# Performance work log

Hardware: AMD Instinct MI355X
Metric: run time of the kernel (lower is better)

## Reference

```python
import jax, jax.numpy as jnp
import numpy as np

N = 100000      # nodes
E = 1600000     # edges
R = 8           # relations
D_IN = 64
D_H = 64
D_OUT = 64
G = 64          # graphs in batch


def setup_inputs() -> dict:
    key = jax.random.key(0)
    ks = jax.random.split(key, 10)
    x = jax.random.normal(ks[0], (N, D_IN), dtype=jnp.float32)
    edge_index = jax.random.randint(ks[1], (2, E), 0, N, dtype=jnp.int32)
    edge_type = jax.random.randint(ks[2], (E,), 0, R, dtype=jnp.int32)
    batch = jnp.sort(jax.random.randint(ks[3], (N,), 0, G, dtype=jnp.int32))
    s1 = 1.0 / np.sqrt(D_IN)
    s2 = 1.0 / np.sqrt(D_H)
    W1 = jax.random.normal(ks[4], (R, D_IN, D_H), dtype=jnp.float32) * s1
    root1 = jax.random.normal(ks[5], (D_IN, D_H), dtype=jnp.float32) * s1
    b1 = jnp.zeros((D_H,), dtype=jnp.float32)
    W2 = jax.random.normal(ks[6], (R, D_H, D_OUT), dtype=jnp.float32) * s2
    root2 = jax.random.normal(ks[7], (D_H, D_OUT), dtype=jnp.float32) * s2
    b2 = jnp.zeros((D_OUT,), dtype=jnp.float32)
    return {"x": x, "edge_index": edge_index, "edge_type": edge_type, "batch": batch,
            "W1": W1, "root1": root1, "b1": b1, "W2": W2, "root2": root2, "b2": b2}


def _rgcn_conv(x, src, dst, etype, W, root, b):
    # PyG RGCNConv (num_bases=None, aggr='mean'):
    #   out_i = sum_r mean_{j in N_r(i)} x_j @ W_r + x_i @ root + b
    # Aggregate-then-transform: per-(dst, relation) mean of source features,
    # then one einsum over relation weights.
    num_nodes, d = x.shape
    num_rel = W.shape[0]
    seg = dst * num_rel + etype                          # composite (node, rel) id
    sums = jax.ops.segment_sum(x[src], seg, num_segments=num_nodes * num_rel)
    cnt = jax.ops.segment_sum(jnp.ones_like(seg, dtype=x.dtype), seg,
                              num_segments=num_nodes * num_rel)
    mean = sums / jnp.maximum(cnt, 1.0)[:, None]         # [N*R, d]
    mean = mean.reshape(num_nodes, num_rel, d)           # [N, R, d]
    return jnp.einsum('nrd,rdh->nh', mean, W) + x @ root + b


def reference(x, edge_index, edge_type, batch, W1, root1, b1, W2, root2, b2):
    src, dst = edge_index[0], edge_index[1]
    h = jax.nn.relu(_rgcn_conv(x, src, dst, edge_type, W1, root1, b1))
    h = _rgcn_conv(h, src, dst, edge_type, W2, root2, b2)
    # global_mean_pool over graph ids
    gsum = jax.ops.segment_sum(h, batch, num_segments=G)
    gcnt = jax.ops.segment_sum(jnp.ones((h.shape[0],), h.dtype), batch, num_segments=G)
    return gsum / jnp.maximum(gcnt, 1.0)[:, None]
```

## Files before the change

kernel.cpp:

```cpp
#include <hip/hip_runtime.h>
#include <stdint.h>

typedef __attribute__((ext_vector_type(8))) short short8;
typedef __attribute__((ext_vector_type(4))) float floatx4;

__device__ inline float bf2f(unsigned short u) {
  union { unsigned int i; float f; } v; v.i = ((unsigned int)u) << 16; return v.f;
}
__device__ inline unsigned short f2bf(float f) {
  union { float f; unsigned int i; } v; v.f = f;
  unsigned int r = v.i + 0x7FFFu + ((v.i >> 16) & 1u);
  return (unsigned short)(r >> 16);
}

__global__ void zero_i32(int* __restrict__ p, int n) {
  int i = blockIdx.x * blockDim.x + threadIdx.x;
  if (i < n) p[i] = 0;
}

__global__ void count_rank(const int* __restrict__ dst, const int* __restrict__ et,
                           int* __restrict__ cnt, unsigned short* __restrict__ rank,
                           int E) {
  int e = blockIdx.x * blockDim.x + threadIdx.x;
  if (e < E) {
    int idx = dst[e] * 8 + et[e];
    rank[e] = (unsigned short)atomicAdd(&cnt[idx], 1);
  }
}

__global__ void invert_cnt(const int* __restrict__ cnt, float* __restrict__ inv, int n) {
  int i = blockIdx.x * blockDim.x + threadIdx.x;
  if (i < n) inv[i] = 1.0f / fmaxf((float)cnt[i], 1.0f);
}

#define SCAN_T 256
#define SCAN_E 4

__global__ void scan1(const int* __restrict__ cnt, int* __restrict__ bsum, int n) {
  __shared__ int lds[SCAN_T];
  int base = blockIdx.x * (SCAN_T * SCAN_E);
  int tid = threadIdx.x;
  int s = 0;
#pragma unroll
  for (int j = 0; j < SCAN_E; ++j) {
    int i = base + tid * SCAN_E + j;
    if (i < n) s += cnt[i];
  }
  lds[tid] = s; __syncthreads();
  for (int off = SCAN_T / 2; off > 0; off >>= 1) {
    if (tid < off) lds[tid] += lds[tid + off];
    __syncthreads();
  }
  if (tid == 0) bsum[blockIdx.x] = lds[0];
}

__global__ void scan2(int* __restrict__ bsum, int* __restrict__ eptr, int nb, int n) {
  __shared__ int lds[SCAN_T];
  int tid = threadIdx.x;
  int loc[4]; int s = 0;
#pragma unroll
  for (int j = 0; j < 4; ++j) {
    int i = tid * 4 + j;
    loc[j] = (i < nb) ? bsum[i] : 0; s += loc[j];
  }
  lds[tid] = s; __syncthreads();
  for (int off = 1; off < SCAN_T; off <<= 1) {
    int v = (tid >= off) ? lds[tid - off] : 0;
    __syncthreads();
    lds[tid] += v;
    __syncthreads();
  }
  int run = (tid > 0 ? lds[tid - 1] : 0);
#pragma unroll
  for (int j = 0; j < 4; ++j) {
    int i = tid * 4 + j;
    if (i < nb) { int v = loc[j]; bsum[i] = run; run += v; }
  }
  if (tid == 0) eptr[n] = lds[SCAN_T - 1];
}

__global__ void scan3(const int* __restrict__ cnt, const int* __restrict__ bsum,
                      int* __restrict__ eptr, int n) {
  __shared__ int lds[SCAN_T];
  int base = blockIdx.x * (SCAN_T * SCAN_E);
  int tid = threadIdx.x;
  int loc[SCAN_E]; int s = 0;
#pragma unroll
  for (int j = 0; j < SCAN_E; ++j) {
    int i = base + tid * SCAN_E + j;
    loc[j] = (i < n) ? cnt[i] : 0; s += loc[j];
  }
  lds[tid] = s; __syncthreads();
  for (int off = 1; off < SCAN_T; off <<= 1) {
    int v = (tid >= off) ? lds[tid - off] : 0;
    __syncthreads();
    lds[tid] += v;
    __syncthreads();
  }
  int run = (tid > 0 ? lds[tid - 1] : 0) + bsum[blockIdx.x];
#pragma unroll
  for (int j = 0; j < SCAN_E; ++j) {
    int i = base + tid * SCAN_E + j;
    if (i < n) { eptr[i] = run; run += loc[j]; }
  }
}

__global__ void scatter_edges(const int* __restrict__ src, const int* __restrict__ dst,
                              const int* __restrict__ et, const int* __restrict__ eptr8,
                              const unsigned short* __restrict__ rank,
                              unsigned* __restrict__ entry, int E) {
  int e = blockIdx.x * blockDim.x + threadIdx.x;
  if (e < E) {
    int d = dst[e], r = et[e];
    int p = eptr8[d * 8 + r] + (int)rank[e];
    entry[p] = ((unsigned)src[e] << 3) | (unsigned)r;
  }
}

__global__ void conv_weights(const float* __restrict__ W, const float* __restrict__ root,
                             unsigned short* __restrict__ Wb, int R) {
  int i = blockIdx.x * blockDim.x + threadIdx.x;
  int total = (R + 1) * 4096;
  if (i >= total) return;
  int m = i >> 12, rem = i & 4095, k = rem >> 6, c = rem & 63;
  float w = (m < R) ? W[(size_t)m * 4096 + k * 64 + c] : root[(size_t)k * 64 + c];
  int kc = k >> 5, q = (k >> 3) & 3, j = k & 7, nt = c >> 4, lcv = c & 15;
  Wb[(size_t)m * 4096 + (size_t)(((kc * 4 + q) * 4 + nt) * 16 + lcv) * 8 + j] = f2bf(w);
}

__global__ void __launch_bounds__(256)
transform_fused(const float* __restrict__ X, const unsigned short* __restrict__ Wb,
                const float* __restrict__ bias, unsigned short* __restrict__ Y,
                float* __restrict__ acc, int N, int relu_in)
{
  const int gy   = blockIdx.y;
  const int base = gy ? 4 : 0;
  const int ng   = gy ? 5 : 4;
  __shared__ __align__(16) unsigned short wlds[5 * 4096];

  const unsigned short* wsrc = Wb + (size_t)base * 4096;
  const int nel = ng * 4096;
  for (int i = threadIdx.x * 8; i < nel; i += 256 * 8)
    *(uint4*)&wlds[i] = *(const uint4*)&wsrc[i];
  __syncthreads();

  const int lane = threadIdx.x & 63;
  const int wave = threadIdx.x >> 6;
  const int lc   = lane & 15;
  const int quad = lane >> 4;
  const int tiles  = (N + 15) >> 4;
  const int stride = gridDim.x * 4;

  for (int t = blockIdx.x * 4 + wave; t < tiles; t += stride) {
    const int nb  = t << 4;
    const int row = min(nb + lc, N - 1);
    const float* xr = X + (size_t)row * 64;
    short8 a0, a1;
#pragma unroll
    for (int j = 0; j < 8; ++j) {
      float v0 = xr[quad * 8 + j];
      float v1 = xr[32 + quad * 8 + j];
      if (relu_in) { v0 = fmaxf(v0, 0.f); v1 = fmaxf(v1, 0.f); }
      a0[j] = (short)f2bf(v0);
      a1[j] = (short)f2bf(v1);
    }
    for (int gi = 0; gi < ng; ++gi) {
      const int g = base + gi;
#pragma unroll
      for (int nt = 0; nt < 4; ++nt) {
        short8 b0 = *(const short8*)&wlds[gi * 4096 + (((0 * 4 + quad) * 4 + nt) * 16 + lc) * 8];
        short8 b1 = *(const short8*)&wlds[gi * 4096 + (((1 * 4 + quad) * 4 + nt) * 16 + lc) * 8];
        floatx4 d = {0.f, 0.f, 0.f, 0.f};
        d = __builtin_amdgcn_mfma_f32_16x16x32_bf16(a0, b0, d, 0, 0, 0);
        d = __builtin_amdgcn_mfma_f32_16x16x32_bf16(a1, b1, d, 0, 0, 0);
        const int c = nt * 16 + lc;
        if (g < 8) {
#pragma unroll
          for (int i = 0; i < 4; ++i) {
            int r_ = nb + quad * 4 + i;
            if (r_ < N) Y[(size_t)r_ * 512 + g * 64 + c] = f2bf(d[i]);
          }
        } else {
          float bv = bias[c];
#pragma unroll
          for (int i = 0; i < 4; ++i) {
            int r_ = nb + quad * 4 + i;
            if (r_ < N) acc[(size_t)r_ * 64 + c] = d[i] + bv;
          }
        }
      }
    }
  }
}

__global__ void __launch_bounds__(256)
edge_agg_csr(const unsigned short* __restrict__ Y, const int* __restrict__ eptr8,
             const unsigned* __restrict__ entry, const float* __restrict__ inv,
             float* __restrict__ acc, int N)
{
  const int wid  = (blockIdx.x * blockDim.x + threadIdx.x) >> 6;
  const int lane = threadIdx.x & 63;
  if (wid >= N) return;
  const int lo = eptr8[wid * 8], hi = eptr8[wid * 8 + 8];
  const float invv = inv[(size_t)wid * 8 + (lane & 7)];
  float sum = 0.f;
  int e = lo;
  for (; e + 4 <= hi; e += 4) {
    unsigned en0 = entry[e], en1 = entry[e + 1], en2 = entry[e + 2], en3 = entry[e + 3];
    float v0 = bf2f(Y[(size_t)(en0 >> 3) * 512 + (en0 & 7) * 64 + lane]);
    float v1 = bf2f(Y[(size_t)(en1 >> 3) * 512 + (en1 & 7) * 64 + lane]);
    float v2 = bf2f(Y[(size_t)(en2 >> 3) * 512 + (en2 & 7) * 64 + lane]);
    float v3 = bf2f(Y[(size_t)(en3 >> 3) * 512 + (en3 & 7) * 64 + lane]);
    sum += v0 * __shfl(invv, (int)(en0 & 7)) + v1 * __shfl(invv, (int)(en1 & 7))
         + v2 * __shfl(invv, (int)(en2 & 7)) + v3 * __shfl(invv, (int)(en3 & 7));
  }
  for (; e < hi; ++e) {
    unsigned en = entry[e];
    float v = bf2f(Y[(size_t)(en >> 3) * 512 + (en & 7) * 64 + lane]);
    sum += v * __shfl(invv, (int)(en & 7));
  }
  acc[(size_t)wid * 64 + lane] += sum;
}

__global__ void glo_bounds(const int* __restrict__ batch, int* __restrict__ glo,
                           int N, int G) {
  int g = blockIdx.x * blockDim.x + threadIdx.x;
  if (g > G) return;
  if (g == G) { glo[G] = N; return; }
  int lo = 0, hi = N;
  while (lo < hi) { int mid = (lo + hi) >> 1; if (batch[mid] < g) lo = mid + 1; else hi = mid; }
  glo[g] = lo;
}

#define PS 24
__global__ void __launch_bounds__(256)
pool1(const float* __restrict__ acc, const int* __restrict__ glo,
      float* __restrict__ partial, int G)
{
  const int g = blockIdx.x;
  const int s = blockIdx.y;
  const int lane = threadIdx.x & 63;
  const int w = threadIdx.x >> 6;
  const int lo = glo[g], hi = glo[g + 1];
  const int len = hi - lo;
  const int a = lo + (int)(((long long)len * s) / PS);
  const int b = lo + (int)(((long long)len * (s + 1)) / PS);
  float sum = 0.f;
  for (int n = a + w; n < b; n += 4) sum += acc[(size_t)n * 64 + lane];
  __shared__ float red[4][64];
  red[w][lane] = sum;
  __syncthreads();
  if (w == 0)
    partial[((size_t)g * PS + s) * 64 + lane] =
        red[0][lane] + red[1][lane] + red[2][lane] + red[3][lane];
}

__global__ void pool2(const float* __restrict__ partial, const int* __restrict__ glo,
                      float* __restrict__ out, int G)
{
  const int g = blockIdx.x;
  const int lane = threadIdx.x;
  float t = 0.f;
#pragma unroll
  for (int s = 0; s < PS; ++s) t += partial[((size_t)g * PS + s) * 64 + lane];
  const int len = glo[g + 1] - glo[g];
  out[(size_t)g * 64 + lane] = t / fmaxf((float)len, 1.0f);
}

extern "C" void kernel_launch(void* const* d_in, const int* in_sizes, int n_in,
                              void* d_out, int out_size, void* d_ws, size_t ws_size,
                              hipStream_t stream)
{
  const float* x     = (const float*)d_in[0];
  const int*   ei    = (const int*)d_in[1];
  const int*   etype = (const int*)d_in[2];
  const int*   batch = (const int*)d_in[3];
  const float* W1    = (const float*)d_in[4];
  const float* root1 = (const float*)d_in[5];
  const float* b1    = (const float*)d_in[6];
  const float* W2    = (const float*)d_in[7];
  const float* root2 = (const float*)d_in[8];
  const float* b2    = (const float*)d_in[9];

  const int N = in_sizes[0] / 64;
  const int E = in_sizes[1] / 2;
  const int R = in_sizes[4] / (64 * 64);
  const int G = out_size / 64;
  const int* srcp = ei;
  const int* dstp = ei + E;
  const int n2 = N * R;

  char* ws = (char*)d_ws;
  size_t off = 0;
  auto carve = [&](size_t bytes) -> void* {
    void* p = ws + off; off = (off + bytes + 255) & ~(size_t)255; return p;
  };
  float*          inv     = (float*)carve((size_t)n2 * 4);
  float*          accA    = (float*)carve((size_t)N * 64 * 4);
  float*          accB    = (float*)carve((size_t)N * 64 * 4);
  unsigned short* Y       = (unsigned short*)carve((size_t)N * R * 64 * 2);
  int*            eptr8   = (int*)carve((size_t)(n2 + 1) * 4);
  unsigned*       entry   = (unsigned*)carve((size_t)E * 4);
  int*            bsum    = (int*)carve(1024 * 4);
  int*            glo     = (int*)carve((size_t)(G + 1) * 4);
  float*          partial = (float*)carve((size_t)G * PS * 64 * 4);
  unsigned short* Wb      = (unsigned short*)carve((size_t)(R + 1) * 4096 * 2);
  unsigned short* rank = (unsigned short*)accA;
  int*            cnt  = (int*)accB;
  (void)ws_size; (void)n_in;

  const int nb2 = (n2 + SCAN_T * SCAN_E - 1) / (SCAN_T * SCAN_E);

  zero_i32<<<(n2 + 255) / 256, 256, 0, stream>>>(cnt, n2);
  count_rank<<<(E + 255) / 256, 256, 0, stream>>>(dstp, etype, cnt, rank, E);
  invert_cnt<<<(n2 + 255) / 256, 256, 0, stream>>>(cnt, inv, n2);
  scan1<<<nb2, SCAN_T, 0, stream>>>(cnt, bsum, n2);
  scan2<<<1, SCAN_T, 0, stream>>>(bsum, eptr8, nb2, n2);
  scan3<<<nb2, SCAN_T, 0, stream>>>(cnt, bsum, eptr8, n2);
  scatter_edges<<<(E + 255) / 256, 256, 0, stream>>>(srcp, dstp, etype, eptr8, rank, entry, E);

  const int tiles = (N + 15) >> 4;
  dim3 tgrid((tiles + 3) / 4, 2);
  const int aggBlocks = (N * 64 + 255) / 256;
  const int wblocks = ((R + 1) * 4096 + 255) / 256;

  conv_weights<<<wblocks, 256, 0, stream>>>(W1, root1, Wb, R);
  transform_fused<<<tgrid, 256, 0, stream>>>(x, Wb, b1, Y, accA, N, 0);
  edge_agg_csr<<<aggBlocks, 256, 0, stream>>>(Y, eptr8, entry, inv, accA, N);

  conv_weights<<<wblocks, 256, 0, stream>>>(W2, root2, Wb, R);
  transform_fused<<<tgrid, 256, 0, stream>>>(accA, Wb, b2, Y, accB, N, 1);
  edge_agg_csr<<<aggBlocks, 256, 0, stream>>>(Y, eptr8, entry, inv, accB, N);

  glo_bounds<<<1, 128, 0, stream>>>(batch, glo, N, G);
  dim3 pgrid(G, PS);
  pool1<<<pgrid, 256, 0, stream>>>(accB, glo, partial, G);
  pool2<<<G, 64, 0, stream>>>(partial, glo, (float*)d_out, G);
}
```

Measured before the change: 463.6 us.

## Switch to aggregate-then-transform with fused gather and MFMA per tile

Replaces the transform-then-gather scheme, which wrote an N×8×64 bf16 per-relation projection and then gathered from it, with a single fused kernel per layer. Each wave gathers bf16 source rows per (node, relation), applies the mean scaling, stages the result in LDS and runs MFMA against the relation weights plus the root term. Input features are converted to bf16 once and layer 1 emits bf16 ReLU output, so the gathered row shrinks from a slice of a 512-wide row to 64 elements. The costs are per-relation serial loops with divergent edge counts, weights now read from global memory instead of LDS, and an extra bf16 rounding of the aggregated means.

```diff
diff --git a/kernel.cpp b/kernel.cpp
--- a/kernel.cpp
+++ b/kernel.cpp
@@ -3,6 +3,7 @@
 
 typedef __attribute__((ext_vector_type(8))) short short8;
 typedef __attribute__((ext_vector_type(4))) float floatx4;
+typedef __attribute__((ext_vector_type(4))) unsigned short ushort4v;
 
 __device__ inline float bf2f(unsigned short u) {
   union { unsigned int i; float f; } v; v.i = ((unsigned int)u) << 16; return v.f;
@@ -16,6 +17,15 @@
 __global__ void zero_i32(int* __restrict__ p, int n) {
   int i = blockIdx.x * blockDim.x + threadIdx.x;
   if (i < n) p[i] = 0;
+}
+
+__global__ void conv_x(const float* __restrict__ X, unsigned short* __restrict__ xb, int n4) {
+  int i = blockIdx.x * blockDim.x + threadIdx.x;
+  if (i < n4) {
+    float4 v = *(const float4*)&X[i * 4];
+    ushort4v o = { f2bf(v.x), f2bf(v.y), f2bf(v.z), f2bf(v.w) };
+    *(ushort4v*)&xb[i * 4] = o;
+  }
 }
 
 __global__ void count_rank(const int* __restrict__ dst, const int* __restrict__ et,
@@ -113,7 +123,7 @@
   if (e < E) {
     int d = dst[e], r = et[e];
     int p = eptr8[d * 8 + r] + (int)rank[e];
-    entry[p] = ((unsigned)src[e] << 3) | (unsigned)r;
+    entry[p] = (unsigned)src[e];
   }
 }
 
@@ -129,97 +139,97 @@
 }
 
 __global__ void __launch_bounds__(256)
-transform_fused(const float* __restrict__ X, const unsigned short* __restrict__ Wb,
-                const float* __restrict__ bias, unsigned short* __restrict__ Y,
-                float* __restrict__ acc, int N, int relu_in)
+rgcn_fused(const unsigned short* __restrict__ xb, const unsigned short* __restrict__ Wb,
+           const float* __restrict__ bias, const int* __restrict__ eptr8,
+           const unsigned* __restrict__ entry, const float* __restrict__ inv,
+           unsigned short* __restrict__ hb, float* __restrict__ acc,
+           int N, int mode)
 {
-  const int gy   = blockIdx.y;
-  const int base = gy ? 4 : 0;
-  const int ng   = gy ? 5 : 4;
-  __shared__ __align__(16) unsigned short wlds[5 * 4096];
-
-  const unsigned short* wsrc = Wb + (size_t)base * 4096;
-  const int nel = ng * 4096;
-  for (int i = threadIdx.x * 8; i < nel; i += 256 * 8)
-    *(uint4*)&wlds[i] = *(const uint4*)&wsrc[i];
-  __syncthreads();
+  __shared__ __align__(16) unsigned short atile[4 * 4096];
 
   const int lane = threadIdx.x & 63;
   const int wave = threadIdx.x >> 6;
   const int lc   = lane & 15;
   const int quad = lane >> 4;
-  const int tiles  = (N + 15) >> 4;
-  const int stride = gridDim.x * 4;
-
-  for (int t = blockIdx.x * 4 + wave; t < tiles; t += stride) {
-    const int nb  = t << 4;
+  const int tiles = (N + 15) >> 4;
+  const int t = blockIdx.x * 4 + wave;
+  if (t >= tiles) return;
+  const int nb = t << 4;
+
+  const int aw    = wave * 4096;
+  const int wbase = aw + ((lane >> 3) * 128) + (lane & 7);
+  const int wx    = (lane >> 3) * 16;
+
+  floatx4 dacc[4];
+#pragma unroll
+  for (int nt = 0; nt < 4; ++nt) dacc[nt] = (floatx4){0.f, 0.f, 0.f, 0.f};
+
+  for (int h = 0; h < 2; ++h) {
+    const int h4 = h * 4;
+    for (int ni = 0; ni < 16; ++ni) {
+      const int d = nb + ni;
+      const int base = d * 8 + h4;
+      const int b0 = eptr8[base],     b1 = eptr8[base + 1];
+      const int b2 = eptr8[base + 2], b3 = eptr8[base + 3], b4 = eptr8[base + 4];
+      const float4 iq = *(const float4*)&inv[base];
+      float s0 = 0.f, s1 = 0.f, s2 = 0.f, s3 = 0.f;
+      int e0 = b0, e1 = b1, e2 = b2, e3 = b3;
+      while ((e0 < b1) | (e1 < b2) | (e2 < b3) | (e3 < b4)) {
+        if (e0 < b1) s0 += bf2f(xb[(size_t)entry[e0++] * 64 + lane]);
+        if (e1 < b2) s1 += bf2f(xb[(size_t)entry[e1++] * 64 + lane]);
+        if (e2 < b3) s2 += bf2f(xb[(size_t)entry[e2++] * 64 + lane]);
+        if (e3 < b4) s3 += bf2f(xb[(size_t)entry[e3++] * 64 + lane]);
+      }
+      const int wsl = wbase + ((ni * 8) ^ wx);
+      atile[wsl]        = f2bf(s0 * iq.x);
+      atile[wsl + 1024] = f2bf(s1 * iq.y);
+      atile[wsl + 2048] = f2bf(s2 * iq.z);
+      atile[wsl + 3072] = f2bf(s3 * iq.w);
+    }
+#pragma unroll
+    for (int kc = 0; kc < 8; ++kc) {
+      const int m = h4 + (kc >> 1);
+      const short8 af = *(const short8*)&atile[aw + (kc * 4 + quad) * 128 +
+                                               ((lc * 8) ^ (((kc & 1) * 4 + quad) * 16))];
+#pragma unroll
+      for (int nt = 0; nt < 4; ++nt) {
+        const short8 bf = *(const short8*)&Wb[(size_t)m * 4096 +
+            (size_t)((((kc & 1) * 4 + quad) * 4 + nt) * 16 + lc) * 8];
+        dacc[nt] = __builtin_amdgcn_mfma_f32_16x16x32_bf16(af, bf, dacc[nt], 0, 0, 0);
+      }
+    }
+  }
+  {
     const int row = min(nb + lc, N - 1);
-    const float* xr = X + (size_t)row * 64;
-    short8 a0, a1;
-#pragma unroll
-    for (int j = 0; j < 8; ++j) {
-      float v0 = xr[quad * 8 + j];
-      float v1 = xr[32 + quad * 8 + j];
-      if (relu_in) { v0 = fmaxf(v0, 0.f); v1 = fmaxf(v1, 0.f); }
-      a0[j] = (short)f2bf(v0);
-      a1[j] = (short)f2bf(v1);
+#pragma unroll
+    for (int kc2 = 0; kc2 < 2; ++kc2) {
+      const short8 af = *(const short8*)&xb[(size_t)row * 64 + kc2 * 32 + quad * 8];
+#pragma unroll
+      for (int nt = 0; nt < 4; ++nt) {
+        const short8 bf = *(const short8*)&Wb[(size_t)8 * 4096 +
+            (size_t)(((kc2 * 4 + quad) * 4 + nt) * 16 + lc) * 8];
+        dacc[nt] = __builtin_amdgcn_mfma_f32_16x16x32_bf16(af, bf, dacc[nt], 0, 0, 0);
+      }
     }
-    for (int gi = 0; gi < ng; ++gi) {
-      const int g = base + gi;
-#pragma unroll
-      for (int nt = 0; nt < 4; ++nt) {
-        short8 b0 = *(const short8*)&wlds[gi * 4096 + (((0 * 4 + quad) * 4 + nt) * 16 + lc) * 8];
-        short8 b1 = *(const short8*)&wlds[gi * 4096 + (((1 * 4 + quad) * 4 + nt) * 16 + lc) * 8];
-        floatx4 d = {0.f, 0.f, 0.f, 0.f};
-        d = __builtin_amdgcn_mfma_f32_16x16x32_bf16(a0, b0, d, 0, 0, 0);
-        d = __builtin_amdgcn_mfma_f32_16x16x32_bf16(a1, b1, d, 0, 0, 0);
-        const int c = nt * 16 + lc;
-        if (g < 8) {
-#pragma unroll
-          for (int i = 0; i < 4; ++i) {
-            int r_ = nb + quad * 4 + i;
-            if (r_ < N) Y[(size_t)r_ * 512 + g * 64 + c] = f2bf(d[i]);
-          }
-        } else {
-          float bv = bias[c];
-#pragma unroll
-          for (int i = 0; i < 4; ++i) {
-            int r_ = nb + quad * 4 + i;
-            if (r_ < N) acc[(size_t)r_ * 64 + c] = d[i] + bv;
-          }
-        }
+  }
+#pragma unroll
+  for (int nt = 0; nt < 4; ++nt) {
+    const int c = nt * 16 + lc;
+    const float bv = bias[c];
+    if (mode) {
+#pragma unroll
+      for (int i = 0; i < 4; ++i) {
+        int r_ = nb + quad * 4 + i;
+        if (r_ < N) hb[(size_t)r_ * 64 + c] = f2bf(fmaxf(dacc[nt][i] + bv, 0.f));
+      }
+    } else {
+#pragma unroll
+      for (int i = 0; i < 4; ++i) {
+        int r_ = nb + quad * 4 + i;
+        if (r_ < N) acc[(size_t)r_ * 64 + c] = dacc[nt][i] + bv;
       }
     }
   }
-}
-
-__global__ void __launch_bounds__(256)
-edge_agg_csr(const unsigned short* __restrict__ Y, const int* __restrict__ eptr8,
-             const unsigned* __restrict__ entry, const float* __restrict__ inv,
-             float* __restrict__ acc, int N)
-{
-  const int wid  = (blockIdx.x * blockDim.x + threadIdx.x) >> 6;
-  const int lane = threadIdx.x & 63;
-  if (wid >= N) return;
-  const int lo = eptr8[wid * 8], hi = eptr8[wid * 8 + 8];
-  const float invv = inv[(size_t)wid * 8 + (lane & 7)];
-  float sum = 0.f;
-  int e = lo;
-  for (; e + 4 <= hi; e += 4) {
-    unsigned en0 = entry[e], en1 = entry[e + 1], en2 = entry[e + 2], en3 = entry[e + 3];
-    float v0 = bf2f(Y[(size_t)(en0 >> 3) * 512 + (en0 & 7) * 64 + lane]);
-    float v1 = bf2f(Y[(size_t)(en1 >> 3) * 512 + (en1 & 7) * 64 + lane]);
-    float v2 = bf2f(Y[(size_t)(en2 >> 3) * 512 + (en2 & 7) * 64 + lane]);
-    float v3 = bf2f(Y[(size_t)(en3 >> 3) * 512 + (en3 & 7) * 64 + lane]);
-    sum += v0 * __shfl(invv, (int)(en0 & 7)) + v1 * __shfl(invv, (int)(en1 & 7))
-         + v2 * __shfl(invv, (int)(en2 & 7)) + v3 * __shfl(invv, (int)(en3 & 7));
-  }
-  for (; e < hi; ++e) {
-    unsigned en = entry[e];
-    float v = bf2f(Y[(size_t)(en >> 3) * 512 + (en & 7) * 64 + lane]);
-    sum += v * __shfl(invv, (int)(en & 7));
-  }
-  acc[(size_t)wid * 64 + lane] += sum;
 }
 
 __global__ void glo_bounds(const int* __restrict__ batch, int* __restrict__ glo,
@@ -296,17 +306,17 @@
     void* p = ws + off; off = (off + bytes + 255) & ~(size_t)255; return p;
   };
   float*          inv     = (float*)carve((size_t)n2 * 4);
-  float*          accA    = (float*)carve((size_t)N * 64 * 4);
-  float*          accB    = (float*)carve((size_t)N * 64 * 4);
-  unsigned short* Y       = (unsigned short*)carve((size_t)N * R * 64 * 2);
+  unsigned short* xb      = (unsigned short*)carve((size_t)N * 64 * 2);
+  unsigned short* hb      = (unsigned short*)carve((size_t)N * 64 * 2);
+  float*          acc     = (float*)carve((size_t)N * 64 * 4);
   int*            eptr8   = (int*)carve((size_t)(n2 + 1) * 4);
   unsigned*       entry   = (unsigned*)carve((size_t)E * 4);
+  unsigned short* rank    = (unsigned short*)carve((size_t)E * 2);
+  int*            cnt     = (int*)carve((size_t)n2 * 4);
   int*            bsum    = (int*)carve(1024 * 4);
   int*            glo     = (int*)carve((size_t)(G + 1) * 4);
   float*          partial = (float*)carve((size_t)G * PS * 64 * 4);
   unsigned short* Wb      = (unsigned short*)carve((size_t)(R + 1) * 4096 * 2);
-  unsigned short* rank = (unsigned short*)accA;
-  int*            cnt  = (int*)accB;
   (void)ws_size; (void)n_in;
 
   const int nb2 = (n2 + SCAN_T * SCAN_E - 1) / (SCAN_T * SCAN_E);
@@ -320,20 +330,19 @@
   scatter_edges<<<(E + 255) / 256, 256, 0, stream>>>(srcp, dstp, etype, eptr8, rank, entry, E);
 
   const int tiles = (N + 15) >> 4;
-  dim3 tgrid((tiles + 3) / 4, 2);
-  const int aggBlocks = (N * 64 + 255) / 256;
+  const int fblocks = (tiles + 3) / 4;
   const int wblocks = ((R + 1) * 4096 + 255) / 256;
 
+  conv_x<<<(N * 64 / 4 + 255) / 256, 256, 0, stream>>>(x, xb, N * 64 / 4);
+
   conv_weights<<<wblocks, 256, 0, stream>>>(W1, root1, Wb, R);
-  transform_fused<<<tgrid, 256, 0, stream>>>(x, Wb, b1, Y, accA, N, 0);
-  edge_agg_csr<<<aggBlocks, 256, 0, stream>>>(Y, eptr8, entry, inv, accA, N);
+  rgcn_fused<<<fblocks, 256, 0, stream>>>(xb, Wb, b1, eptr8, entry, inv, hb, nullptr, N, 1);
 
   conv_weights<<<wblocks, 256, 0, stream>>>(W2, root2, Wb, R);
-  transform_fused<<<tgrid, 256, 0, stream>>>(accA, Wb, b2, Y, accB, N, 1);
-  edge_agg_csr<<<aggBlocks, 256, 0, stream>>>(Y, eptr8, entry, inv, accB, N);
+  rgcn_fused<<<fblocks, 256, 0, stream>>>(hb, Wb, b2, eptr8, entry, inv, nullptr, acc, N, 0);
 
   glo_bounds<<<1, 128, 0, stream>>>(batch, glo, N, G);
   dim3 pgrid(G, PS);
-  pool1<<<pgrid, 256, 0, stream>>>(accB, glo, partial, G);
+  pool1<<<pgrid, 256, 0, stream>>>(acc, glo, partial, G);
   pool2<<<G, 64, 0, stream>>>(partial, glo, (float*)d_out, G);
 }
```

After: 888.5 us. +91.7%, slower.
